# Performance work log

Measured on AMD Instinct MI355X. Metric: run time of the kernel, lower is better.

Reference implementation:

```python
import jax, jax.numpy as jnp
import numpy as np

ENERGY = 0.4  # target low-frequency energy ratio (ctor default energy=0.4)


def setup_inputs() -> dict:
    key = jax.random.key(0)
    x = jax.random.normal(key, (8, 64, 256, 256), dtype=jnp.float32)
    return {"x": x}


def _min_cutoff_map(H, W):
    """For each pixel of the fftshifted spectrum, the smallest cutoff c such that
    the pixel lies inside the central box [crow-c:crow+c, ccol-c:ccol+c].
    A pixel (r, cc) is inside iff c >= max(-dr, dr+1) and c >= max(-dc, dc+1)."""
    crow, ccol = H // 2, W // 2
    dr = np.arange(H) - crow
    dc = np.arange(W) - ccol
    mr = np.maximum(-dr, dr + 1)
    mc = np.maximum(-dc, dc + 1)
    return np.maximum(mr[:, None], mc[None, :]).astype(np.int32)  # [H, W]


def reference(x):
    B, C, H, W = x.shape
    # fp32 FFT (matches the autocast-disabled fft in the original)
    fshift = jnp.fft.fftshift(jnp.fft.fft2(x.astype(jnp.float32)), axes=(-2, -1))

    minc = jnp.asarray(_min_cutoff_map(H, W))          # [H, W] int32
    nseg = max(H // 2, W // 2) + 1                      # static
    K = min(H, W) // 2                                  # candidates are 1..K-1

    # Radial (box) cumulative energy profile of channel 0, one pass per sample.
    mag2 = jnp.abs(fshift[:, 0]) ** 2                   # [B, H, W]
    ids = minc.reshape(-1)
    per_box = jax.vmap(
        lambda m: jax.ops.segment_sum(m.reshape(-1), ids, num_segments=nseg)
    )(mag2)                                             # [B, nseg]
    cum = jnp.cumsum(per_box, axis=-1)                  # cum[b, c] = box-energy at cutoff c
    total = cum[:, -1]
    target = ENERGY * total

    found = cum[:, 1:K] >= target[:, None]              # candidates c = 1..K-1
    first = jnp.argmax(found, axis=-1) + 1              # smallest satisfying c
    cutoff = jnp.where(jnp.any(found, axis=-1), first, 5)  # fallback 5, as in torch

    # Zero the central box per sample (broadcast over channels), then inverse FFT.
    keep = (minc[None, None, :, :] > cutoff[:, None, None, None]).astype(jnp.float32)
    hp = fshift * keep
    out = jnp.abs(jnp.fft.ifft2(jnp.fft.ifftshift(hp, axes=(-2, -1))))
    return out
```

## Files before the change

kernel.cpp:

```cpp
#include <hip/hip_runtime.h>
#include <hip/hip_fp16.h>
#include <math.h>

#define RESERVE 16384

__device__ __forceinline__ float2 cadd(float2 a, float2 b){ return make_float2(a.x+b.x, a.y+b.y); }
__device__ __forceinline__ float2 csub(float2 a, float2 b){ return make_float2(a.x-b.x, a.y-b.y); }
__device__ __forceinline__ float2 cmul(float2 a, float2 b){ return make_float2(a.x*b.x - a.y*b.y, a.x*b.y + a.y*b.x); }
__device__ __forceinline__ float2 cmulc(float2 a, float2 b){
  return make_float2(a.x*b.x + a.y*b.y, a.x*b.y - a.y*b.x); }
__device__ __forceinline__ __half2 f2h(float2 v){ return __floats2half2_rn(v.x, v.y); }
__device__ __forceinline__ float2 h2f(__half2 h){ return __half22float2(h); }

#define SCHED_FENCE() __builtin_amdgcn_sched_barrier(0x7F)

__device__ __forceinline__ constexpr int rho4(int r) { return ((r & 3) << 2) | (r >> 2); }

template<int DIR> __device__ __forceinline__ float2 twc(float2 z, float c, float s) {
  const float si = (DIR < 0) ? s : -s;
  return make_float2(c*z.x - si*z.y, c*z.y + si*z.x);
}
template<int DIR> __device__ __forceinline__ float2 mulmi(float2 z) {
  return (DIR < 0) ? make_float2(z.y, -z.x) : make_float2(-z.y, z.x);
}

template<int DIR, bool REV>
__device__ __forceinline__ void fft16(float2* v) {
  #define IX(i) (REV ? rho4(i) : (i))
  #pragma unroll
  for (int j0 = 0; j0 < 4; ++j0) {
    float2 a0 = v[IX(j0)], a1 = v[IX(j0+4)], a2 = v[IX(j0+8)], a3 = v[IX(j0+12)];
    float2 t0 = cadd(a0,a2), t1 = csub(a0,a2), t2 = cadd(a1,a3), d = csub(a1,a3);
    float2 t3 = (DIR < 0) ? make_float2(d.y,-d.x) : make_float2(-d.y,d.x);
    v[IX(j0)]    = cadd(t0,t2);
    v[IX(j0+4)]  = cadd(t1,t3);
    v[IX(j0+8)]  = csub(t0,t2);
    v[IX(j0+12)] = csub(t1,t3);
  }
  v[IX(5)]  = twc<DIR>(v[IX(5)],  0.92387953f, -0.38268343f);
  v[IX(6)]  = twc<DIR>(v[IX(6)],  0.70710678f, -0.70710678f);
  v[IX(7)]  = twc<DIR>(v[IX(7)],  0.38268343f, -0.92387953f);
  v[IX(9)]  = twc<DIR>(v[IX(9)],  0.70710678f, -0.70710678f);
  v[IX(10)] = mulmi<DIR>(v[IX(10)]);
  v[IX(11)] = twc<DIR>(v[IX(11)], -0.70710678f, -0.70710678f);
  v[IX(13)] = twc<DIR>(v[IX(13)],  0.38268343f, -0.92387953f);
  v[IX(14)] = twc<DIR>(v[IX(14)], -0.70710678f, -0.70710678f);
  v[IX(15)] = twc<DIR>(v[IX(15)], -0.92387953f,  0.38268343f);
  #pragma unroll
  for (int k1 = 0; k1 < 4; ++k1) {
    float2 a0 = v[IX(4*k1)], a1 = v[IX(4*k1+1)], a2 = v[IX(4*k1+2)], a3 = v[IX(4*k1+3)];
    float2 t0 = cadd(a0,a2), t1 = csub(a0,a2), t2 = cadd(a1,a3), d = csub(a1,a3);
    float2 t3 = (DIR < 0) ? make_float2(d.y,-d.x) : make_float2(-d.y,d.x);
    v[IX(4*k1)]   = cadd(t0,t2);
    v[IX(4*k1+1)] = cadd(t1,t3);
    v[IX(4*k1+2)] = csub(t0,t2);
    v[IX(4*k1+3)] = csub(t1,t3);
  }
  #undef IX
}

__device__ __forceinline__ void make_twf(int l, float2* twf) {
  float s, c;
  sincospif((float)l * (-1.0f/128.0f), &s, &c);
  const float2 w = make_float2(c, s);
  twf[0] = make_float2(1.f, 0.f);
  #pragma unroll
  for (int k = 1; k < 16; ++k) twf[k] = cmul(twf[k-1], w);
}

template<int DIR, bool REV1, bool HB>
__device__ __forceinline__ void fft256g(float2* v, void* trb, int l, const float2* twf) {
  fft16<DIR, REV1>(v);
  if (HB) {
    __half2* t = (__half2*)trb;
    #pragma unroll
    for (int r = 0; r < 16; ++r) {
      const int k1 = REV1 ? r : rho4(r);
      float2 z = v[r];
      z = (DIR < 0) ? cmul(twf[k1], z) : cmulc(twf[k1], z);
      t[k1 * 17 + l] = f2h(z);
    }
    SCHED_FENCE();
    #pragma unroll
    for (int j = 0; j < 16; ++j) v[j] = h2f(t[l * 17 + j]);
  } else {
    float2* t = (float2*)trb;
    #pragma unroll
    for (int r = 0; r < 16; ++r) {
      const int k1 = REV1 ? r : rho4(r);
      float2 z = v[r];
      z = (DIR < 0) ? cmul(twf[k1], z) : cmulc(twf[k1], z);
      t[k1 * 17 + l] = z;
    }
    SCHED_FENCE();
    #pragma unroll
    for (int j = 0; j < 16; ++j) v[j] = ((float2*)trb)[l * 17 + j];
  }
  SCHED_FENCE();
  fft16<DIR, false>(v);
}

#define GS32 276
#define GS16 280

__global__ __launch_bounds__(256) void k_pass1(const float* __restrict__ x,
    __half2* __restrict__ Bt, int img0, int istep) {
  __shared__ __align__(16) char smraw[16 * GS32 * 8];
  float2*  trb  = (float2*)smraw;
  __half2* tile = (__half2*)smraw;
  const int tid = threadIdx.x, g = tid >> 4, l = tid & 15;
  const int slot = blockIdx.y, img = img0 + slot * istep;
  const int row = (blockIdx.x << 4) + g;
  const float* xr = x + ((size_t)img << 16) + (row << 8);
  float rv[16];
  #pragma unroll
  for (int j = 0; j < 16; ++j) rv[j] = xr[l + (j << 4)];
  float2 twf[16]; make_twf(l, twf);
  float2 v[16];
  #pragma unroll
  for (int j = 0; j < 16; ++j) v[j] = make_float2(rv[j], 0.f);
  fft256g<-1, false, false>(v, trb + g * GS32, l, twf);
  __syncthreads();
  #pragma unroll
  for (int rr = 0; rr < 16; ++rr)
    tile[(l + (rho4(rr) << 4)) * 17 + g] = f2h(v[rr]);
  __syncthreads();
  __half2* bo = Bt + ((size_t)slot << 16) + (blockIdx.x << 4);
  const int rloc = tid & 15, ub = tid >> 4;
  #pragma unroll
  for (int jj = 0; jj < 16; ++jj) {
    const int u = (jj << 4) + ub;
    bo[(u << 8) + rloc] = tile[u * 17 + rloc];
  }
}

__global__ __launch_bounds__(256) void k_pass2(const __half2* __restrict__ Bt,
    __half2* __restrict__ Ct, const int* __restrict__ cutoffs, int img0, int istep) {
  __shared__ __align__(16) char smraw[16 * GS16 * 4];
  __half2* trb  = (__half2*)smraw;
  __half2* tile = (__half2*)smraw;
  const int tid = threadIdx.x, g = tid >> 4, l = tid & 15;
  const int slot = blockIdx.y, img = img0 + slot * istep;
  const int u = (blockIdx.x << 4) + g;
  const __half2* col = Bt + ((size_t)slot << 16) + (u << 8);
  __half2 hv[16];
  #pragma unroll
  for (int j = 0; j < 16; ++j) hv[j] = col[l + (j << 4)];
  const int cut = cutoffs[img >> 6];
  float2 twf[16]; make_twf(l, twf);
  float2 v[16];
  #pragma unroll
  for (int j = 0; j < 16; ++j) v[j] = h2f(hv[j]);
  fft256g<-1, false, true>(v, trb + g * GS16, l, twf);
  if ((u < cut) | (u >= 256 - cut)) {
    #pragma unroll
    for (int rr = 0; rr < 16; ++rr) {
      const int vi = l + (rho4(rr) << 4);
      if (vi < cut || vi >= 256 - cut) v[rr] = make_float2(0.f, 0.f);
    }
  }
  fft256g<1, true, true>(v, trb + g * GS16, l, twf);
  __syncthreads();
  #pragma unroll
  for (int rr = 0; rr < 16; ++rr)
    tile[(l + (rho4(rr) << 4)) * 17 + g] = f2h(v[rr]);
  __syncthreads();
  __half2* co = Ct + ((size_t)slot << 16) + (blockIdx.x << 4);
  const int cloc = tid & 15, rb = tid >> 4;
  #pragma unroll
  for (int jj = 0; jj < 16; ++jj) {
    const int r = (jj << 4) + rb;
    co[(r << 8) + cloc] = tile[r * 17 + cloc];
  }
}

__global__ __launch_bounds__(256) void k_pass3(const __half2* __restrict__ Ct,
    float* __restrict__ out, int img0, int istep) {
  __shared__ __half2 trbs[16 * GS16];
  const int tid = threadIdx.x, g = tid >> 4, l = tid & 15;
  const int slot = blockIdx.y, img = img0 + slot * istep;
  float2 twf[16]; make_twf(l, twf);
  #pragma unroll
  for (int k = 0; k < 16; ++k) { twf[k].x *= 0.0625f; twf[k].y *= 0.0625f; }
  const __half2* cim = Ct + ((size_t)slot << 16);
  float* oim = out + ((size_t)img << 16);
  __half2* tb = trbs + g * GS16;
  #pragma unroll 1
  for (int it = 0; it < 4; ++it) {
    const int row = (blockIdx.x << 6) + (it << 4) + g;
    const __half2* rp = cim + (row << 8);
    float2 v[16];
    #pragma unroll
    for (int j = 0; j < 16; ++j) v[j] = h2f(rp[l + (j << 4)]);
    fft256g<1, false, true>(v, tb, l, twf);
    float* orow = oim + (row << 8);
    #pragma unroll
    for (int rr = 0; rr < 16; ++rr) {
      const float2 z = v[rr];
      orow[l + (rho4(rr) << 4)] = __builtin_amdgcn_sqrtf(z.x*z.x + z.y*z.y) * (1.f/4096.f);
    }
  }
}

__global__ __launch_bounds__(256) void k_hist(const __half2* __restrict__ Bt,
    double* __restrict__ bins, int slot0, int sstep, int batch0) {
  __shared__ float2 trbuf[16 * GS32];
  __shared__ float whist[4][132];
  const int tid = threadIdx.x, g = tid >> 4, l = tid & 15, wave = tid >> 6;
  const int lb = blockIdx.y;
  const int batch = batch0 + lb;
  const size_t slot = (size_t)(slot0 + lb * sstep);
  const int u = (blockIdx.x << 4) + g;
  float2 twf[16]; make_twf(l, twf);
  for (int i = tid & 63; i < 132; i += 64) whist[wave][i] = 0.f;
  __syncthreads();
  const __half2* col = Bt + (slot << 16) + (u << 8);
  float2 v[16];
  #pragma unroll
  for (int j = 0; j < 16; ++j) v[j] = h2f(col[l + (j << 4)]);
  fft256g<-1, false, false>(v, trbuf + g * GS32, l, twf);
  const int fc = (u < 128) ? u + 1 : 256 - u;
  #pragma unroll
  for (int rr = 0; rr < 16; ++rr) {
    const int vi = l + (rho4(rr) << 4);
    const int fu = (vi < 128) ? vi + 1 : 256 - vi;
    const int seg = fu > fc ? fu : fc;
    const float2 z = v[rr];
    atomicAdd(&whist[wave][seg], z.x*z.x + z.y*z.y);
  }
  __syncthreads();
  for (int s = tid; s < 129; s += 256) {
    const float sum = whist[0][s] + whist[1][s] + whist[2][s] + whist[3][s];
    if (sum != 0.f) atomicAdd(&bins[batch * 129 + s], (double)sum);
  }
}

__global__ void k_cutoff(const double* __restrict__ bins, int* __restrict__ cutoffs) {
  const int b = threadIdx.x;
  if (b < 8) {
    const double* Bv = bins + b * 129;
    double total = 0.0;
    for (int s = 0; s < 129; ++s) total += Bv[s];
    const double target = 0.4 * total;
    double cum = Bv[0];
    int cut = 5;
    bool found = false;
    for (int s = 1; s <= 127; ++s) {
      cum += Bv[s];
      if (!found && cum >= target) { cut = s; found = true; }
    }
    cutoffs[b] = cut;
  }
}

extern "C" void kernel_launch(void* const* d_in, const int* in_sizes, int n_in,
                              void* d_out, int out_size, void* d_ws, size_t ws_size,
                              hipStream_t stream) {
  const float* x = (const float*)d_in[0];
  float* out = (float*)d_out;
  char* wsb = (char*)d_ws;
  double* bins    = (double*)wsb;
  int*    cutoffs = (int*)(wsb + 8448);
  char*   payload = wsb + RESERVE;

  size_t avail = (ws_size > RESERVE) ? ws_size - (size_t)RESERVE : 0;
  long long Gl = (long long)(avail / 524288);
  int G = (Gl > 512) ? 512 : (int)Gl;
  if (G < 1) G = 1;
  __half2* Bt = (__half2*)payload;
  __half2* Ct = (__half2*)(payload + (size_t)G * 262144);

  hipMemsetAsync(bins, 0, 8 * 129 * sizeof(double), stream);
  dim3 blk(256, 1, 1);

  if (G >= 512) {
    k_pass1<<<dim3(16, 512), blk, 0, stream>>>(x, Bt, 0, 1);
    k_hist <<<dim3(16, 8),   blk, 0, stream>>>(Bt, bins, 0, 64, 0);
    k_cutoff<<<dim3(1), dim3(64), 0, stream>>>(bins, cutoffs);
    k_pass2<<<dim3(16, 512), blk, 0, stream>>>(Bt, Ct, cutoffs, 0, 1);
    k_pass3<<<dim3(4, 512),  blk, 0, stream>>>(Ct, out, 0, 1);
  } else {
    int Gp = G > 8 ? 8 : G;
    for (int b0 = 0; b0 < 8; b0 += Gp) {
      int n = (8 - b0 < Gp) ? (8 - b0) : Gp;
      k_pass1<<<dim3(16, n), blk, 0, stream>>>(x, Bt, b0 * 64, 64);
      k_hist <<<dim3(16, n), blk, 0, stream>>>(Bt, bins, 0, 1, b0);
    }
    k_cutoff<<<dim3(1), dim3(64), 0, stream>>>(bins, cutoffs);
    for (int g0 = 0; g0 < 512; g0 += G) {
      int n = (512 - g0 < G) ? (512 - g0) : G;
      k_pass1<<<dim3(16, n), blk, 0, stream>>>(x, Bt, g0, 1);
      k_pass2<<<dim3(16, n), blk, 0, stream>>>(Bt, Ct, cutoffs, g0, 1);
      k_pass3<<<dim3(4, n),  blk, 0, stream>>>(Ct, out, g0, 1);
    }
  }
}
```

Before: 227.2 us.

## Tile intermediate spectra layout and stage global I/O through swizzled LDS

Changes the intermediate Bt/Ct layout from strided column tiles to contiguous 16x16 blocks, so every kernel reads and writes global memory with 16-byte vectorised, coalesced accesses staged through XOR-swizzled shared memory. Pass1 and pass3 now load and store whole row tiles with float4, replacing per-element strided accesses. Pass3 now handles 16 rows per block over 16 blocks instead of looping over 64 rows. The cost is more shared memory per block and extra barriers, which may lower occupancy.

```diff
diff --git a/kernel.cpp b/kernel.cpp
--- a/kernel.cpp
+++ b/kernel.cpp
@@ -103,55 +103,83 @@
 #define GS32 276
 #define GS16 280
 
+__device__ __forceinline__ int SW(int row, int col) {
+  return (row << 8) + (col ^ ((row & 7) << 2) ^ ((row & 1) << 4));
+}
+__device__ __forceinline__ int SW16(int r, int ul) {
+  return (r << 4) + (ul ^ (r & 14));
+}
+
+
 __global__ __launch_bounds__(256) void k_pass1(const float* __restrict__ x,
     __half2* __restrict__ Bt, int img0, int istep) {
-  __shared__ __align__(16) char smraw[16 * GS32 * 8];
-  float2*  trb  = (float2*)smraw;
-  __half2* tile = (__half2*)smraw;
+  __shared__ __align__(16) char smraw[16384];
+  __shared__ __align__(16) float2 trbf[16 * GS32];
+  float*   rowstage = (float*)smraw;
+  __half2* outtile  = (__half2*)smraw;
   const int tid = threadIdx.x, g = tid >> 4, l = tid & 15;
   const int slot = blockIdx.y, img = img0 + slot * istep;
-  const int row = (blockIdx.x << 4) + g;
-  const float* xr = x + ((size_t)img << 16) + (row << 8);
-  float rv[16];
-  #pragma unroll
-  for (int j = 0; j < 16; ++j) rv[j] = xr[l + (j << 4)];
+  const int r0 = blockIdx.x << 4;
   float2 twf[16]; make_twf(l, twf);
+  const float* xsrc = x + ((size_t)img << 16) + (r0 << 8);
+  #pragma unroll
+  for (int it = 0; it < 4; ++it) {
+    const int L = it * 1024 + tid * 4;
+    const float4 d = *reinterpret_cast<const float4*>(xsrc + L);
+    *reinterpret_cast<float4*>(rowstage + SW(L >> 8, L & 255)) = d;
+  }
+  __syncthreads();
   float2 v[16];
   #pragma unroll
-  for (int j = 0; j < 16; ++j) v[j] = make_float2(rv[j], 0.f);
-  fft256g<-1, false, false>(v, trb + g * GS32, l, twf);
-  __syncthreads();
+  for (int j = 0; j < 16; ++j)
+    v[j] = make_float2(rowstage[SW(g, l + (j << 4))], 0.f);
+  __syncthreads();
+  fft256g<-1, false, false>(v, trbf + g * GS32, l, twf);
   #pragma unroll
   for (int rr = 0; rr < 16; ++rr)
-    tile[(l + (rho4(rr) << 4)) * 17 + g] = f2h(v[rr]);
-  __syncthreads();
-  __half2* bo = Bt + ((size_t)slot << 16) + (blockIdx.x << 4);
-  const int rloc = tid & 15, ub = tid >> 4;
-  #pragma unroll
-  for (int jj = 0; jj < 16; ++jj) {
-    const int u = (jj << 4) + ub;
-    bo[(u << 8) + rloc] = tile[u * 17 + rloc];
+    outtile[SW(g, l + (rho4(rr) << 4))] = f2h(v[rr]);
+  __syncthreads();
+  __half2* bdst = Bt + ((size_t)slot << 16) + (r0 << 4);
+  #pragma unroll
+  for (int it = 0; it < 4; ++it) {
+    const int L = it * 1024 + tid * 4;
+    const int p = L >> 8, rl = (L >> 4) & 15, ul0 = L & 15;
+    const int4 d = *reinterpret_cast<const int4*>(outtile + SW(rl, (p << 4) + ul0));
+    *reinterpret_cast<int4*>(bdst + (p << 12) + (L & 255)) = d;
   }
 }
 
 __global__ __launch_bounds__(256) void k_pass2(const __half2* __restrict__ Bt,
     __half2* __restrict__ Ct, const int* __restrict__ cutoffs, int img0, int istep) {
-  __shared__ __align__(16) char smraw[16 * GS16 * 4];
-  __half2* trb  = (__half2*)smraw;
-  __half2* tile = (__half2*)smraw;
+  __shared__ __align__(16) char smraw[16384];
+  __shared__ __align__(16) __half2 trbh[16 * GS16];
+  __half2* instage = (__half2*)smraw;
+  __half2* outtile = (__half2*)smraw;
   const int tid = threadIdx.x, g = tid >> 4, l = tid & 15;
   const int slot = blockIdx.y, img = img0 + slot * istep;
-  const int u = (blockIdx.x << 4) + g;
-  const __half2* col = Bt + ((size_t)slot << 16) + (u << 8);
-  __half2 hv[16];
-  #pragma unroll
-  for (int j = 0; j < 16; ++j) hv[j] = col[l + (j << 4)];
+  const int p = blockIdx.x;
   const int cut = cutoffs[img >> 6];
   float2 twf[16]; make_twf(l, twf);
+  const __half2* bsrc = Bt + ((size_t)slot << 16) + (p << 12);
+  #pragma unroll
+  for (int it = 0; it < 4; ++it) {
+    const int L = it * 1024 + tid * 4;
+    const int4 d = *reinterpret_cast<const int4*>(bsrc + L);
+    const int r = L >> 4, ul0 = L & 15;
+    const int i0 = SW16(r, ul0);
+    *reinterpret_cast<int2*>(instage + i0) = make_int2(d.x, d.y);
+    *reinterpret_cast<int2*>(instage + (i0 ^ 2)) = make_int2(d.z, d.w);
+  }
+  __syncthreads();
+  __half2 hv[16];
+  #pragma unroll
+  for (int j = 0; j < 16; ++j) hv[j] = instage[SW16(l + (j << 4), g)];
+  __syncthreads();
+  const int u = (p << 4) + g;
   float2 v[16];
   #pragma unroll
   for (int j = 0; j < 16; ++j) v[j] = h2f(hv[j]);
-  fft256g<-1, false, true>(v, trb + g * GS16, l, twf);
+  fft256g<-1, false, true>(v, trbh + g * GS16, l, twf);
   if ((u < cut) | (u >= 256 - cut)) {
     #pragma unroll
     for (int rr = 0; rr < 16; ++rr) {
@@ -159,66 +187,96 @@
       if (vi < cut || vi >= 256 - cut) v[rr] = make_float2(0.f, 0.f);
     }
   }
-  fft256g<1, true, true>(v, trb + g * GS16, l, twf);
-  __syncthreads();
+  fft256g<1, true, true>(v, trbh + g * GS16, l, twf);
   #pragma unroll
   for (int rr = 0; rr < 16; ++rr)
-    tile[(l + (rho4(rr) << 4)) * 17 + g] = f2h(v[rr]);
-  __syncthreads();
-  __half2* co = Ct + ((size_t)slot << 16) + (blockIdx.x << 4);
-  const int cloc = tid & 15, rb = tid >> 4;
-  #pragma unroll
-  for (int jj = 0; jj < 16; ++jj) {
-    const int r = (jj << 4) + rb;
-    co[(r << 8) + cloc] = tile[r * 17 + cloc];
+    outtile[SW16(l + (rho4(rr) << 4), g)] = f2h(v[rr]);
+  __syncthreads();
+  __half2* cdst = Ct + ((size_t)slot << 16) + (p << 12);
+  #pragma unroll
+  for (int it = 0; it < 4; ++it) {
+    const int L = it * 1024 + tid * 4;
+    const int r = L >> 4, ul0 = L & 15;
+    const int i0 = SW16(r, ul0);
+    const int2 a = *reinterpret_cast<const int2*>(outtile + i0);
+    const int2 b = *reinterpret_cast<const int2*>(outtile + (i0 ^ 2));
+    *reinterpret_cast<int4*>(cdst + L) = make_int4(a.x, a.y, b.x, b.y);
   }
 }
 
 __global__ __launch_bounds__(256) void k_pass3(const __half2* __restrict__ Ct,
     float* __restrict__ out, int img0, int istep) {
-  __shared__ __half2 trbs[16 * GS16];
+  __shared__ __align__(16) char smraw[16384];
+  __shared__ __align__(16) __half2 trbh[16 * GS16];
+  __half2* instage  = (__half2*)smraw;
+  float*   outstage = (float*)smraw;
   const int tid = threadIdx.x, g = tid >> 4, l = tid & 15;
   const int slot = blockIdx.y, img = img0 + slot * istep;
+  const int r0 = blockIdx.x << 4;
   float2 twf[16]; make_twf(l, twf);
   #pragma unroll
   for (int k = 0; k < 16; ++k) { twf[k].x *= 0.0625f; twf[k].y *= 0.0625f; }
-  const __half2* cim = Ct + ((size_t)slot << 16);
-  float* oim = out + ((size_t)img << 16);
-  __half2* tb = trbs + g * GS16;
-  #pragma unroll 1
-  for (int it = 0; it < 4; ++it) {
-    const int row = (blockIdx.x << 6) + (it << 4) + g;
-    const __half2* rp = cim + (row << 8);
-    float2 v[16];
-    #pragma unroll
-    for (int j = 0; j < 16; ++j) v[j] = h2f(rp[l + (j << 4)]);
-    fft256g<1, false, true>(v, tb, l, twf);
-    float* orow = oim + (row << 8);
-    #pragma unroll
-    for (int rr = 0; rr < 16; ++rr) {
-      const float2 z = v[rr];
-      orow[l + (rho4(rr) << 4)] = __builtin_amdgcn_sqrtf(z.x*z.x + z.y*z.y) * (1.f/4096.f);
-    }
+  const __half2* csrc = Ct + ((size_t)slot << 16) + (r0 << 4);
+  #pragma unroll
+  for (int it = 0; it < 4; ++it) {
+    const int L = it * 1024 + tid * 4;
+    const int p = L >> 8, rl = (L >> 4) & 15, ul0 = L & 15;
+    const int4 d = *reinterpret_cast<const int4*>(csrc + (p << 12) + (L & 255));
+    *reinterpret_cast<int4*>(instage + SW(rl, (p << 4) + ul0)) = d;
+  }
+  __syncthreads();
+  __half2 hv[16];
+  #pragma unroll
+  for (int j = 0; j < 16; ++j) hv[j] = instage[SW(g, l + (j << 4))];
+  __syncthreads();
+  float2 v[16];
+  #pragma unroll
+  for (int j = 0; j < 16; ++j) v[j] = h2f(hv[j]);
+  fft256g<1, false, true>(v, trbh + g * GS16, l, twf);
+  #pragma unroll
+  for (int rr = 0; rr < 16; ++rr) {
+    const float2 z = v[rr];
+    outstage[SW(g, l + (rho4(rr) << 4))] =
+        __builtin_amdgcn_sqrtf(z.x*z.x + z.y*z.y) * (1.f/4096.f);
+  }
+  __syncthreads();
+  float* odst = out + ((size_t)img << 16) + (r0 << 8);
+  #pragma unroll
+  for (int it = 0; it < 4; ++it) {
+    const int L = it * 1024 + tid * 4;
+    const float4 d = *reinterpret_cast<const float4*>(outstage + SW(L >> 8, L & 255));
+    *reinterpret_cast<float4*>(odst + L) = d;
   }
 }
 
 __global__ __launch_bounds__(256) void k_hist(const __half2* __restrict__ Bt,
     double* __restrict__ bins, int slot0, int sstep, int batch0) {
-  __shared__ float2 trbuf[16 * GS32];
+  __shared__ __align__(16) __half2 instage[4096];
+  __shared__ __align__(16) float2 trbf[16 * GS32];
   __shared__ float whist[4][132];
   const int tid = threadIdx.x, g = tid >> 4, l = tid & 15, wave = tid >> 6;
   const int lb = blockIdx.y;
   const int batch = batch0 + lb;
   const size_t slot = (size_t)(slot0 + lb * sstep);
-  const int u = (blockIdx.x << 4) + g;
+  const int p = blockIdx.x;
+  const int u = (p << 4) + g;
   float2 twf[16]; make_twf(l, twf);
   for (int i = tid & 63; i < 132; i += 64) whist[wave][i] = 0.f;
-  __syncthreads();
-  const __half2* col = Bt + (slot << 16) + (u << 8);
+  const __half2* bsrc = Bt + (slot << 16) + (p << 12);
+  #pragma unroll
+  for (int it = 0; it < 4; ++it) {
+    const int L = it * 1024 + tid * 4;
+    const int4 d = *reinterpret_cast<const int4*>(bsrc + L);
+    const int r = L >> 4, ul0 = L & 15;
+    const int i0 = SW16(r, ul0);
+    *reinterpret_cast<int2*>(instage + i0) = make_int2(d.x, d.y);
+    *reinterpret_cast<int2*>(instage + (i0 ^ 2)) = make_int2(d.z, d.w);
+  }
+  __syncthreads();
   float2 v[16];
   #pragma unroll
-  for (int j = 0; j < 16; ++j) v[j] = h2f(col[l + (j << 4)]);
-  fft256g<-1, false, false>(v, trbuf + g * GS32, l, twf);
+  for (int j = 0; j < 16; ++j) v[j] = h2f(instage[SW16(l + (j << 4), g)]);
+  fft256g<-1, false, false>(v, trbf + g * GS32, l, twf);
   const int fc = (u < 128) ? u + 1 : 256 - u;
   #pragma unroll
   for (int rr = 0; rr < 16; ++rr) {
@@ -278,7 +336,7 @@
     k_hist <<<dim3(16, 8),   blk, 0, stream>>>(Bt, bins, 0, 64, 0);
     k_cutoff<<<dim3(1), dim3(64), 0, stream>>>(bins, cutoffs);
     k_pass2<<<dim3(16, 512), blk, 0, stream>>>(Bt, Ct, cutoffs, 0, 1);
-    k_pass3<<<dim3(4, 512),  blk, 0, stream>>>(Ct, out, 0, 1);
+    k_pass3<<<dim3(16, 512), blk, 0, stream>>>(Ct, out, 0, 1);
   } else {
     int Gp = G > 8 ? 8 : G;
     for (int b0 = 0; b0 < 8; b0 += Gp) {
@@ -291,7 +349,7 @@
       int n = (512 - g0 < G) ? (512 - g0) : G;
       k_pass1<<<dim3(16, n), blk, 0, stream>>>(x, Bt, g0, 1);
       k_pass2<<<dim3(16, n), blk, 0, stream>>>(Bt, Ct, cutoffs, g0, 1);
-      k_pass3<<<dim3(4, n),  blk, 0, stream>>>(Ct, out, g0, 1);
-    }
-  }
-}
+      k_pass3<<<dim3(16, n), blk, 0, stream>>>(Ct, out, g0, 1);
+    }
+  }
+}
```

Result: faster. 209.8 us (-7.7%).
